# Optimization experiments

Measured on AMD Instinct MI355X. Metric: run time of the kernel, lower is better.

The kernel has to match this reference:

```python
import jax, jax.numpy as jnp
import numpy as np
from jax import lax

_DN = ('NCHW', 'OIHW', 'NCHW')


def _depthwise_kernel(C):
    base = jnp.array([[0.1, 0.1, 0.1], [0.1, 0.2, 0.1], [0.1, 0.1, 0.1]], jnp.float32)
    return jnp.broadcast_to(base[None, None], (C, 1, 3, 3))


def setup_inputs() -> dict:
    key = jax.random.key(0)
    k0, k1, k2 = jax.random.split(key, 3)
    T, B, C, H, W = 16, 16, 8, 128, 128
    hidden = max(1, C // 16)  # reduction_ratio = 16
    events = jax.random.normal(k0, (T, B, C, H, W), jnp.float32)
    conv_w = _depthwise_kernel(C)  # fixed neighbor kernel from _initialize_weights
    att_w1 = jax.random.normal(k1, (hidden, 2 * C), jnp.float32) / np.sqrt(2 * C)
    att_w2 = jax.random.normal(k2, (C, hidden), jnp.float32) / np.sqrt(hidden)
    return {
        'events': events,
        'conv_w': conv_w,
        'att_w1': att_w1,
        'att_w2': att_w2,
        'density_w': jnp.array(1.0, jnp.float32),
        'temporal_w': jnp.array(0.8, jnp.float32),
        'motion_w': jnp.array(0.5, jnp.float32),
    }


def _forward(events, conv_w, att_w1, att_w2, density_w, temporal_w, motion_w):
    T, B, C, H, W = events.shape
    x = events.reshape(T * B, C, H, W)
    # depthwise 3x3 neighbor conv (groups=C), batched over all T steps at once
    wi = lax.conv_general_dilated(x, conv_w, (1, 1), 'SAME',
                                  dimension_numbers=_DN, feature_group_count=C)
    # --- BALIFBetaAdaptor: max/avg pool -> 1x1 convs (== matmuls) -> sigmoid ---
    mx = jnp.max(x, axis=(2, 3))            # (TB, C)
    av = jnp.mean(x, axis=(2, 3))           # (TB, C)
    pooled = jnp.concatenate([mx, av], axis=1)  # (TB, 2C)
    h = jax.nn.relu(pooled @ att_w1.T)
    beta = (0.5 + 0.45 * jax.nn.sigmoid(h @ att_w2.T)).reshape(T, B, C, 1, 1)
    # --- LightweightEventAdaptor: density / temporal change / unfold variance ---
    density = jnp.mean(x, axis=(1, 2, 3)).reshape(T, B)
    diff = jnp.mean(jnp.abs(events[1:] - events[:-1]), axis=(2, 3, 4))
    temporal = jnp.concatenate([jnp.zeros((1, B), events.dtype), diff], axis=0)  # t=0 -> 0
    # F.unfold(k=3,pad=1) variance over dim=1 (C*9 values, unbiased) via sum-convs
    ones_k = jnp.ones((1, C, 3, 3), events.dtype)
    s1 = lax.conv_general_dilated(x, ones_k, (1, 1), 'SAME', dimension_numbers=_DN)
    s2 = lax.conv_general_dilated(x * x, ones_k, (1, 1), 'SAME', dimension_numbers=_DN)
    n = C * 9
    var = (s2 - s1 * s1 / n) / (n - 1)      # (TB,1,H,W), matches torch.var (ddof=1)
    motion = jnp.mean(var, axis=(1, 2, 3)).reshape(T, B)
    adj = jax.nn.sigmoid(density_w * density + temporal_w * temporal + motion_w * motion) * 2.0
    thr = (1.0 + adj).reshape(T, B, 1, 1, 1)  # base_threshold = 1.0
    wi = wi.reshape(T, B, C, H, W)

    # --- sequential LIF charge/fire/reset (torch.no_grad -> stop_gradient) ---
    def step(v, inp):
        w, b, th, cur = inp
        v = lax.stop_gradient(b * v + (1.0 - b) * w)              # charge
        spike = lax.stop_gradient(jnp.arctan(2.0 * (v - th)) * 0.5 + 0.5)  # atan surrogate
        v = lax.stop_gradient((1.0 - spike) * v)                  # reset (v_reset = 0)
        return v, cur * spike

    v0 = jnp.zeros((B, C, H, W), events.dtype)
    _, out = lax.scan(step, v0, (wi, beta, thr, events))
    return out  # (T,B,C,H,W)


def reference(events, conv_w, att_w1, att_w2, density_w, temporal_w, motion_w):
    return _forward(events, conv_w, att_w1, att_w2, density_w, temporal_w, motion_w)
```

## Files before the change

### kernel.cpp

```cpp
#include <hip/hip_runtime.h>
#include <math.h>

#define T_ 16
#define B_ 16
#define C_ 8
#define H_ 128
#define W_ 128
#define HW_ (H_*W_)
#define CHW_ (C_*HW_)
#define NSLICE 4
#define ROWS_PER_SLICE (H_/NSLICE)
#define NV 19

__device__ __forceinline__ float wave_sum(float v){
    #pragma unroll
    for (int o=32;o>0;o>>=1) v += __shfl_down(v,o,64);
    return v;
}
__device__ __forceinline__ float wave_max(float v){
    #pragma unroll
    for (int o=32;o>0;o>>=1) v = fmaxf(v,__shfl_down(v,o,64));
    return v;
}

__global__ __launch_bounds__(128) void stats_kernel(
    const float* __restrict__ events, float* __restrict__ partials)
{
    int blk = blockIdx.x;
    int s  = blk % NSLICE;
    int tb = blk / NSLICE;
    int t  = tb / B_;
    int w  = threadIdx.x;
    int h0 = s * ROWS_PER_SLICE;
    const float* frame = events + (size_t)tb * CHW_;
    const float* prev  = frame - (size_t)B_ * CHW_;

    __shared__ float yb[ROWS_PER_SLICE+2][W_];

    float maxc[C_], sumc[C_];
    #pragma unroll
    for (int c=0;c<C_;c++){ maxc[c] = -INFINITY; sumc[c] = 0.f; }
    float dsum=0.f, m1=0.f, m2=0.f;
    float cntw = (w==0 || w==W_-1) ? 2.f : 3.f;

    for (int r=0; r<ROWS_PER_SLICE+2; ++r){
        int gh = h0 - 1 + r;
        float y = 0.f;
        if (gh >= 0 && gh < H_){
            bool own = (r>=1 && r<=ROWS_PER_SLICE);
            float xv[C_];
            #pragma unroll
            for (int c=0;c<C_;c++){
                float x = frame[c*HW_ + gh*W_ + w];
                xv[c] = x; y += x;
            }
            if (own){
                float ysq = 0.f;
                #pragma unroll
                for (int c=0;c<C_;c++){
                    float x = xv[c];
                    ysq += x*x;
                    maxc[c] = fmaxf(maxc[c], x);
                    sumc[c] += x;
                }
                float cnth = (gh==0 || gh==H_-1) ? 2.f : 3.f;
                m2 += ysq * cnth * cntw;
                if (t > 0){
                    #pragma unroll
                    for (int c=0;c<C_;c++)
                        dsum += fabsf(xv[c] - prev[c*HW_ + gh*W_ + w]);
                }
            }
        }
        yb[r][w] = y;
    }
    __syncthreads();

    for (int r=1; r<=ROWS_PER_SLICE; ++r){
        float s1 = 0.f;
        #pragma unroll
        for (int dr=-1; dr<=1; ++dr){
            const float* row = yb[r+dr];
            float v = row[w];
            if (w>0)      v += row[w-1];
            if (w<W_-1)   v += row[w+1];
            s1 += v;
        }
        m1 += s1*s1;
    }

    float vals[NV];
    #pragma unroll
    for (int c=0;c<C_;c++){ vals[c]=sumc[c]; vals[8+c]=maxc[c]; }
    vals[16]=dsum; vals[17]=m1; vals[18]=m2;

    __shared__ float red[2][NV];
    int lane = w & 63, wv = w >> 6;
    #pragma unroll
    for (int i=0;i<NV;i++){
        float r = (i>=8 && i<16) ? wave_max(vals[i]) : wave_sum(vals[i]);
        if (lane==0) red[wv][i] = r;
    }
    __syncthreads();
    if (w < NV){
        float a = red[0][w], b = red[1][w];
        float r = (w>=8 && w<16) ? fmaxf(a,b) : (a+b);
        partials[((size_t)tb*NSLICE + s)*NV + w] = r;
    }
}

__global__ __launch_bounds__(64) void combine_kernel(
    const float* __restrict__ partials,
    const float* __restrict__ att_w1,
    const float* __restrict__ att_w2,
    const float* __restrict__ dwp, const float* __restrict__ twp,
    const float* __restrict__ mwp,
    float* __restrict__ beta_out, float* __restrict__ thr_out,
    float* __restrict__ zeropad)
{
    int tb = blockIdx.x;
    int t  = tb / B_;
    int i  = threadIdx.x;
    if (tb == 0 && i < 16) zeropad[i] = 0.f;
    __shared__ float v[NV];
    if (i < NV){
        const float* p = partials + (size_t)tb*NSLICE*NV;
        float a = p[i], b = p[NV+i], c = p[2*NV+i], d = p[3*NV+i];
        v[i] = (i>=8 && i<16) ? fmaxf(fmaxf(a,b),fmaxf(c,d)) : (a+b+c+d);
    }
    __syncthreads();
    if (i == 0){
        float h1 = 0.f;
        for (int c=0;c<C_;c++) h1 += v[8+c] * att_w1[c];
        for (int c=0;c<C_;c++) h1 += (v[c]/(float)HW_) * att_w1[C_+c];
        h1 = fmaxf(h1, 0.f);
        float total = 0.f;
        for (int c=0;c<C_;c++) total += v[c];
        float density  = total / (float)CHW_;
        float temporal = (t==0) ? 0.f : v[16] / (float)CHW_;
        float motion   = (v[18] - v[17]/72.f) / 71.f / (float)HW_;
        float z = dwp[0]*density + twp[0]*temporal + mwp[0]*motion;
        float adj = 2.f / (1.f + expf(-z));
        thr_out[tb] = 1.f + adj;
        for (int c=0;c<C_;c++){
            float sg = 1.f / (1.f + expf(-(h1 * att_w2[c])));
            beta_out[tb*C_ + c] = 0.5f + 0.45f*sg;
        }
    }
}


__device__ __forceinline__ void gload16(const float* src, float* lds_dst){
    __builtin_amdgcn_global_load_lds(
        (const __attribute__((address_space(1))) unsigned int*)src,
        (__attribute__((address_space(3))) unsigned int*)lds_dst, 16, 0, 0);
}

__device__ __forceinline__ float fast_atan(float x){
    float ax = fabsf(x);
    bool inv = ax > 1.f;
    float z  = inv ? __builtin_amdgcn_rcpf(ax) : ax;
    float z2 = z*z;
    float p = -0.0117212f;
    p = fmaf(p, z2,  0.05265332f);
    p = fmaf(p, z2, -0.11643287f);
    p = fmaf(p, z2,  0.19354346f);
    p = fmaf(p, z2, -0.33262347f);
    p = fmaf(p, z2,  0.99997726f);
    p = p * z;
    float r = inv ? (1.57079632679f - p) : p;
    return copysignf(r, x);
}

#define SROWS 10

__global__ __launch_bounds__(256, 8) void lif_kernel(
    const float* __restrict__ events,
    const float* __restrict__ conv_w,
    const float* __restrict__ beta,
    const float* __restrict__ thr,
    const float* __restrict__ zeropad,
    float* __restrict__ out)
{
    int bid  = blockIdx.x;
    int hblk = bid & 15;
    int bc   = bid >> 4;
    int b = bc >> 3, c = bc & 7;
    int h0 = hblk * 8;
    int tid = threadIdx.x;
    int wv  = tid >> 6;

    float wk[9];
    #pragma unroll
    for (int k=0;k<9;k++) wk[k] = conv_w[c*9 + k];

    __shared__ float lds[2][SROWS*W_];

    int idxA = tid,        rowA = idxA >> 5, colA = (idxA & 31) * 4;
    int idxB = 256 + tid,  rowB = idxB >> 5, colB = (idxB & 31) * 4;
    int ghA = h0 - 1 + rowA;
    int ghB = h0 - 1 + rowB;
    bool okA = (ghA >= 0) && (ghA < H_);
    bool okB = (ghB >= 0) && (ghB < H_);
    const float* baseFrame = events + ((size_t)(b * C_) + c) * HW_;
    const float* srcA0 = okA ? (baseFrame + ghA*W_ + colA) : zeropad;
    const float* srcB0 = okB ? (baseFrame + ghB*W_ + colB) : zeropad;
    const size_t tstep = (size_t)B_ * CHW_;
    size_t stepA = okA ? tstep : 0;
    size_t stepB = okB ? tstep : 0;

    int w  = tid & 127;
    int rg = tid >> 7;
    int rbase = rg * 4;
    int wl = (w > 0)    ? w-1 : 0;
    int wr = (w < W_-1) ? w+1 : W_-1;
    bool hasL = (w > 0), hasR = (w < W_-1);

    float v[4];
    #pragma unroll
    for (int i=0;i<4;i++) v[i] = 0.f;

    gload16(srcA0, &lds[0][wv*256]);
    if (wv == 0) gload16(srcB0, &lds[0][1024]);

    const float* bp = beta + (b*C_ + c);
    const float* tp = thr + b;
    float bv = bp[0];
    float th = tp[0];

    for (int t = 0; t < T_; ++t){
        int cur = t & 1, nxt = cur ^ 1;
        __syncthreads();

        if (t + 1 < T_){
            gload16(srcA0 + (size_t)(t+1)*stepA, &lds[nxt][wv*256]);
            if (wv == 0) gload16(srcB0 + (size_t)(t+1)*stepB, &lds[nxt][1024]);
        }
        float bvn = (t+1 < T_) ? bp[(size_t)(t+1)*B_*C_] : 0.f;
        float thn = (t+1 < T_) ? tp[(size_t)(t+1)*B_]    : 0.f;

        const float* L = &lds[cur][0];
        float omb = 1.f - bv;
        float* op = out + ((size_t)(t*B_+b)*C_ + c)*HW_ + h0*W_;

        const float* row0 = L + rbase*W_;
        const float* row1 = row0 + W_;
        float la = hasL ? row0[wl] : 0.f;  float ma = row0[w];  float ra = hasR ? row0[wr] : 0.f;
        float lb = hasL ? row1[wl] : 0.f;  float mb = row1[w];  float rb = hasR ? row1[wr] : 0.f;

        #pragma unroll
        for (int i=0;i<4;i++){
            const float* rowc = L + (rbase+2+i)*W_;
            float lc = hasL ? rowc[wl] : 0.f;
            float mc = rowc[w];
            float rc = hasR ? rowc[wr] : 0.f;
            float wi = wk[0]*la + wk[1]*ma + wk[2]*ra
                     + wk[3]*lb + wk[4]*mb + wk[5]*rb
                     + wk[6]*lc + wk[7]*mc + wk[8]*rc;
            float vv = fmaf(bv, v[i], omb*wi);
            float sp = fast_atan(2.f*(vv - th))*0.5f + 0.5f;
            op[(rbase+i)*W_ + w] = mb * sp;
            v[i] = (1.f - sp) * vv;
            la=lb; ma=mb; ra=rb; lb=lc; mb=mc; rb=rc;
        }
        bv = bvn; th = thn;
    }
}

extern "C" void kernel_launch(void* const* d_in, const int* in_sizes, int n_in,
                              void* d_out, int out_size, void* d_ws, size_t ws_size,
                              hipStream_t stream)
{
    const float* events = (const float*)d_in[0];
    const float* conv_w = (const float*)d_in[1];
    const float* att_w1 = (const float*)d_in[2];
    const float* att_w2 = (const float*)d_in[3];
    const float* dwp    = (const float*)d_in[4];
    const float* twp    = (const float*)d_in[5];
    const float* mwp    = (const float*)d_in[6];
    float* out = (float*)d_out;

    float* ws       = (float*)d_ws;
    float* partials = ws;
    float* beta     = ws + (size_t)T_*B_*NSLICE*NV;
    float* thr      = beta + (size_t)T_*B_*C_;
    float* zeropad  = thr + T_*B_;

    stats_kernel  <<<T_*B_*NSLICE, 128, 0, stream>>>(events, partials);
    combine_kernel<<<T_*B_,        64,  0, stream>>>(partials, att_w1, att_w2,
                                                     dwp, twp, mwp, beta, thr, zeropad);
    lif_kernel    <<<B_*C_*16,     256, 0, stream>>>(events, conv_w, beta, thr, zeropad, out);
}
```

Baseline: 96.12 us.

## Restructure stats kernel with float4 loads, more slices, and 256-thread blocks

The stats kernel now splits each frame into 8 row slices instead of 4 and runs 256 threads per block. Each thread loads float4 vectors covering 4 columns and handles two rows, and halo rows are loaded separately by the first two waves. The 3x3 box-sum pass now reuses row sums in a sliding window, and the combine kernel loops over NSLICE partials. The aim is more memory-level parallelism and wider loads for the stats read of the full events tensor, at the cost of more halo reloads and more partials.

```diff
diff --git a/kernel.cpp b/kernel.cpp
--- a/kernel.cpp
+++ b/kernel.cpp
@@ -8,8 +8,8 @@
 #define W_ 128
 #define HW_ (H_*W_)
 #define CHW_ (C_*HW_)
-#define NSLICE 4
-#define ROWS_PER_SLICE (H_/NSLICE)
+#define NSLICE 8
+#define SR (H_/NSLICE)
 #define NV 19
 
 __device__ __forceinline__ float wave_sum(float v){
@@ -23,70 +23,106 @@
     return v;
 }
 
-__global__ __launch_bounds__(128) void stats_kernel(
+__global__ __launch_bounds__(256) void stats_kernel(
     const float* __restrict__ events, float* __restrict__ partials)
 {
     int blk = blockIdx.x;
-    int s  = blk % NSLICE;
-    int tb = blk / NSLICE;
-    int t  = tb / B_;
-    int w  = threadIdx.x;
-    int h0 = s * ROWS_PER_SLICE;
+    int s  = blk & (NSLICE-1);
+    int tb = blk >> 3;
+    int t  = tb >> 4;
+    int h0 = s * SR;
+    int tid = threadIdx.x;
     const float* frame = events + (size_t)tb * CHW_;
     const float* prev  = frame - (size_t)B_ * CHW_;
 
-    __shared__ float yb[ROWS_PER_SLICE+2][W_];
-
-    float maxc[C_], sumc[C_];
-    #pragma unroll
-    for (int c=0;c<C_;c++){ maxc[c] = -INFINITY; sumc[c] = 0.f; }
+    __shared__ float yb[SR+2][W_];
+    __shared__ float red[4][NV];
+
+    int cg = tid & 31;
+    int c0 = cg * 4;
+    int r  = tid >> 5;
+
+    float cnt0 = (c0   == 0 || c0   == W_-1) ? 2.f : 3.f;
+    float cnt1 = 3.f;
+    float cnt2 = 3.f;
+    float cnt3 = (c0+3 == 0 || c0+3 == W_-1) ? 2.f : 3.f;
+
+    float sumc[C_], maxc[C_];
+    #pragma unroll
+    for (int c=0;c<C_;c++){ sumc[c]=0.f; maxc[c]=-INFINITY; }
     float dsum=0.f, m1=0.f, m2=0.f;
-    float cntw = (w==0 || w==W_-1) ? 2.f : 3.f;
-
-    for (int r=0; r<ROWS_PER_SLICE+2; ++r){
-        int gh = h0 - 1 + r;
-        float y = 0.f;
+
+    if (tid < 64){
+        int hr = (tid >> 5) ? SR : -1;
+        int gh = h0 + hr;
+        float y0=0.f,y1=0.f,y2=0.f,y3=0.f;
         if (gh >= 0 && gh < H_){
-            bool own = (r>=1 && r<=ROWS_PER_SLICE);
-            float xv[C_];
+            const float* rp = frame + gh*W_ + (tid&31)*4;
             #pragma unroll
             for (int c=0;c<C_;c++){
-                float x = frame[c*HW_ + gh*W_ + w];
-                xv[c] = x; y += x;
+                float4 x = *reinterpret_cast<const float4*>(rp + c*HW_);
+                y0+=x.x; y1+=x.y; y2+=x.z; y3+=x.w;
             }
-            if (own){
-                float ysq = 0.f;
-                #pragma unroll
-                for (int c=0;c<C_;c++){
-                    float x = xv[c];
-                    ysq += x*x;
-                    maxc[c] = fmaxf(maxc[c], x);
-                    sumc[c] += x;
-                }
-                float cnth = (gh==0 || gh==H_-1) ? 2.f : 3.f;
-                m2 += ysq * cnth * cntw;
-                if (t > 0){
-                    #pragma unroll
-                    for (int c=0;c<C_;c++)
-                        dsum += fabsf(xv[c] - prev[c*HW_ + gh*W_ + w]);
-                }
+        }
+        float* yp = &yb[hr+1][(tid&31)*4];
+        yp[0]=y0; yp[1]=y1; yp[2]=y2; yp[3]=y3;
+    }
+
+    #pragma unroll 1
+    for (int p=0;p<2;p++){
+        int lr = r + 8*p;
+        int gh = h0 + lr;
+        const float* rp = frame + gh*W_ + c0;
+        float4 xv[C_];
+        #pragma unroll
+        for (int c=0;c<C_;c++)
+            xv[c] = *reinterpret_cast<const float4*>(rp + c*HW_);
+
+        float y0=0.f,y1=0.f,y2=0.f,y3=0.f;
+        float q0=0.f,q1=0.f,q2=0.f,q3=0.f;
+        #pragma unroll
+        for (int c=0;c<C_;c++){
+            float4 x = xv[c];
+            y0+=x.x; y1+=x.y; y2+=x.z; y3+=x.w;
+            q0=fmaf(x.x,x.x,q0); q1=fmaf(x.y,x.y,q1);
+            q2=fmaf(x.z,x.z,q2); q3=fmaf(x.w,x.w,q3);
+            sumc[c] += (x.x+x.y)+(x.z+x.w);
+            maxc[c] = fmaxf(maxc[c], fmaxf(fmaxf(x.x,x.y),fmaxf(x.z,x.w)));
+        }
+        float cnth = (gh==0 || gh==H_-1) ? 2.f : 3.f;
+        m2 += cnth * (q0*cnt0 + q1*cnt1 + q2*cnt2 + q3*cnt3);
+
+        if (t > 0){
+            const float* pp = prev + gh*W_ + c0;
+            #pragma unroll
+            for (int c=0;c<C_;c++){
+                float4 pv = *reinterpret_cast<const float4*>(pp + c*HW_);
+                float4 x  = xv[c];
+                dsum += fabsf(x.x-pv.x)+fabsf(x.y-pv.y)
+                      + fabsf(x.z-pv.z)+fabsf(x.w-pv.w);
             }
         }
-        yb[r][w] = y;
+        float* yp = &yb[lr+1][c0];
+        yp[0]=y0; yp[1]=y1; yp[2]=y2; yp[3]=y3;
     }
     __syncthreads();
 
-    for (int r=1; r<=ROWS_PER_SLICE; ++r){
-        float s1 = 0.f;
-        #pragma unroll
-        for (int dr=-1; dr<=1; ++dr){
-            const float* row = yb[r+dr];
-            float v = row[w];
-            if (w>0)      v += row[w-1];
-            if (w<W_-1)   v += row[w+1];
-            s1 += v;
-        }
-        m1 += s1*s1;
+    {
+        int w  = tid & 127;
+        int rg = tid >> 7;
+        bool hasL = (w>0), hasR = (w<W_-1);
+        int base = rg*8;
+        const float* row;
+        row = yb[base];   float a0 = row[w] + (hasL?row[w-1]:0.f) + (hasR?row[w+1]:0.f);
+        row = yb[base+1]; float a1 = row[w] + (hasL?row[w-1]:0.f) + (hasR?row[w+1]:0.f);
+        #pragma unroll
+        for (int i=0;i<8;i++){
+            row = yb[base+2+i];
+            float a2 = row[w] + (hasL?row[w-1]:0.f) + (hasR?row[w+1]:0.f);
+            float s1 = a0 + a1 + a2;
+            m1 = fmaf(s1, s1, m1);
+            a0 = a1; a1 = a2;
+        }
     }
 
     float vals[NV];
@@ -94,18 +130,17 @@
     for (int c=0;c<C_;c++){ vals[c]=sumc[c]; vals[8+c]=maxc[c]; }
     vals[16]=dsum; vals[17]=m1; vals[18]=m2;
 
-    __shared__ float red[2][NV];
-    int lane = w & 63, wv = w >> 6;
+    int lane = tid & 63, wv = tid >> 6;
     #pragma unroll
     for (int i=0;i<NV;i++){
-        float r = (i>=8 && i<16) ? wave_max(vals[i]) : wave_sum(vals[i]);
-        if (lane==0) red[wv][i] = r;
+        float rr = (i>=8 && i<16) ? wave_max(vals[i]) : wave_sum(vals[i]);
+        if (lane==0) red[wv][i] = rr;
     }
     __syncthreads();
-    if (w < NV){
-        float a = red[0][w], b = red[1][w];
-        float r = (w>=8 && w<16) ? fmaxf(a,b) : (a+b);
-        partials[((size_t)tb*NSLICE + s)*NV + w] = r;
+    if (tid < NV){
+        float a = red[0][tid], b = red[1][tid], c = red[2][tid], d = red[3][tid];
+        float rr = (tid>=8 && tid<16) ? fmaxf(fmaxf(a,b),fmaxf(c,d)) : ((a+b)+(c+d));
+        partials[((size_t)tb*NSLICE + s)*NV + tid] = rr;
     }
 }
 
@@ -125,8 +160,14 @@
     __shared__ float v[NV];
     if (i < NV){
         const float* p = partials + (size_t)tb*NSLICE*NV;
-        float a = p[i], b = p[NV+i], c = p[2*NV+i], d = p[3*NV+i];
-        v[i] = (i>=8 && i<16) ? fmaxf(fmaxf(a,b),fmaxf(c,d)) : (a+b+c+d);
+        bool mx = (i>=8 && i<16);
+        float acc = p[i];
+        #pragma unroll
+        for (int k=1;k<NSLICE;k++){
+            float x = p[k*NV + i];
+            acc = mx ? fmaxf(acc, x) : (acc + x);
+        }
+        v[i] = acc;
     }
     __syncthreads();
     if (i == 0){
@@ -149,7 +190,6 @@
     }
 }
 
-
 __device__ __forceinline__ void gload16(const float* src, float* lds_dst){
     __builtin_amdgcn_global_load_lds(
         (const __attribute__((address_space(1))) unsigned int*)src,
@@ -286,7 +326,7 @@
     float* thr      = beta + (size_t)T_*B_*C_;
     float* zeropad  = thr + T_*B_;
 
-    stats_kernel  <<<T_*B_*NSLICE, 128, 0, stream>>>(events, partials);
+    stats_kernel  <<<T_*B_*NSLICE, 256, 0, stream>>>(events, partials);
     combine_kernel<<<T_*B_,        64,  0, stream>>>(partials, att_w1, att_w2,
                                                      dwp, twp, mwp, beta, thr, zeropad);
     lif_kernel    <<<B_*C_*16,     256, 0, stream>>>(events, conv_w, beta, thr, zeropad, out);
```

New measurement: 94.12 us. 2.1% less time.
